# Kernel tuning notes

Hardware: AMD Instinct MI355X
Metric: run time of the kernel (lower is better)

Reference implementation:

```python
import jax, jax.numpy as jnp
import numpy as np

EMB = 256
N_NODES = 20000
N_EDGES = 200000


def _sage_layer(x, src, dst, edge_attr, W, b, n_nodes):
    # message = x[src] + edge_attr ; mean-aggregate into dst ; ReLU(Linear([x;agg]))
    msg = x[src] + edge_attr                                   # [2E, emb]
    s = jax.ops.segment_sum(msg, dst, num_segments=n_nodes)    # [N, emb]
    cnt = jax.ops.segment_sum(jnp.ones((dst.shape[0], 1), x.dtype), dst,
                              num_segments=n_nodes)            # [N, 1]
    agg = s / jnp.maximum(cnt, 1.0)
    return jax.nn.relu(jnp.concatenate([x, agg], axis=1) @ W + b)


def setup_inputs() -> dict:
    key = jax.random.key(0)
    ks = jax.random.split(key, 12)
    sc = 0.05
    inp = {
        "x": jax.random.normal(ks[0], (N_NODES, EMB), jnp.float32),
        "edge_attr": jax.random.normal(ks[1], (N_EDGES, EMB), jnp.float32),
        "batch_q_embds": jax.random.normal(ks[2], (N_EDGES, EMB), jnp.float32),
        "edge_index": jax.random.randint(ks[3], (2, N_EDGES), 0, N_NODES, jnp.int64
                                         if jax.config.jax_enable_x64 else jnp.int32),
        "W_rev1": jax.random.normal(ks[4], (EMB, EMB), jnp.float32) * sc,
        "b_rev1": jnp.zeros((EMB,), jnp.float32),
        "W_rev2": jax.random.normal(ks[5], (EMB, EMB), jnp.float32) * sc,
        "b_rev2": jnp.zeros((EMB,), jnp.float32),
        "W_sage1": jax.random.normal(ks[6], (2 * EMB, EMB), jnp.float32) * sc,
        "b_sage1": jnp.zeros((EMB,), jnp.float32),
        "W_sage2": jax.random.normal(ks[7], (2 * EMB, EMB), jnp.float32) * sc,
        "b_sage2": jnp.zeros((EMB,), jnp.float32),
        "W_pred1": jax.random.normal(ks[8], (6 * EMB, EMB), jnp.float32) * sc,
        "b_pred1": jnp.zeros((EMB,), jnp.float32),
        "W_pred2": jax.random.normal(ks[9], (EMB, 1), jnp.float32) * sc,
        "b_pred2": jnp.zeros((1,), jnp.float32),
    }
    return inp


def reference(x, edge_attr, batch_q_embds, edge_index,
              W_rev1, b_rev1, W_rev2, b_rev2,
              W_sage1, b_sage1, W_sage2, b_sage2,
              W_pred1, b_pred1, W_pred2, b_pred2):
    src, dst = edge_index[0], edge_index[1]
    # reverse-edge attributes via proj_reverse MLP
    edge_attr_rev = jax.nn.relu(edge_attr @ W_rev1 + b_rev1) @ W_rev2 + b_rev2
    src_f = jnp.concatenate([src, dst])          # [2E]
    dst_f = jnp.concatenate([dst, src])          # [2E]
    ea_f = jnp.concatenate([edge_attr, edge_attr_rev], axis=0)  # [2E, emb]
    # 2-layer GraphSAGE backbone over nodes, collect per-layer outputs
    h1 = _sage_layer(x, src_f, dst_f, ea_f, W_sage1, b_sage1, N_NODES)
    h2 = _sage_layer(h1, src_f, dst_f, ea_f, W_sage2, b_sage2, N_NODES)
    h_e = jnp.concatenate([h1, h2], axis=1)      # [N, 2*emb]
    # per-edge triple features: [q ; h_e[head] ; edge_attr ; h_e[tail]]
    h_triple = jnp.concatenate([batch_q_embds, h_e[src], edge_attr, h_e[dst]], axis=1)
    attn_logits = (jax.nn.relu(h_triple @ W_pred1 + b_pred1) @ W_pred2 + b_pred2)[:, 0]
    # idp-bern sampling (training=True): gumbel-like logistic noise, temp=1
    u = jax.random.uniform(jax.random.key(42), attn_logits.shape,
                           attn_logits.dtype, 1e-10, 1.0 - 1e-10)
    noise = jnp.log(u) - jnp.log(1.0 - u)
    sampled = jax.nn.sigmoid(attn_logits + noise)
    return attn_logits, sampled
```

## Files before the change

### kernel.cpp

```cpp
#include <hip/hip_runtime.h>
#include <cstdint>
#include <cstddef>

#define EMB 256
#define NN 20000
#define NE 200000
#define NE2 400000

typedef unsigned short ushort_t;
typedef __attribute__((ext_vector_type(8))) short bf16x8;
typedef __attribute__((ext_vector_type(4))) float f32x4;

__device__ __forceinline__ ushort_t f2bf(float f) {
    unsigned u = __float_as_uint(f);
    u += 0x7FFFu + ((u >> 16) & 1u);
    return (ushort_t)(u >> 16);
}
__device__ __forceinline__ float bf2f(ushort_t u) {
    return __uint_as_float(((unsigned)u) << 16);
}

__device__ __forceinline__ void async_cp16(const ushort_t* g, ushort_t* l) {
    __builtin_amdgcn_global_load_lds(
        (const __attribute__((address_space(1))) unsigned int*)g,
        (__attribute__((address_space(3))) unsigned int*)l,
        16, 0, 0);
}

__device__ __forceinline__ unsigned rotl32(unsigned v, int d) {
    return (v << d) | (v >> (32 - d));
}
__device__ __forceinline__ void threefry2x32(unsigned k0, unsigned k1,
                                             unsigned x0, unsigned x1,
                                             unsigned& o0, unsigned& o1) {
    unsigned k2 = k0 ^ k1 ^ 0x1BD11BDAu;
    x0 += k0; x1 += k1;
#define TF_R(r) { x0 += x1; x1 = rotl32(x1, (r)); x1 ^= x0; }
    TF_R(13) TF_R(15) TF_R(26) TF_R(6)
    x0 += k1; x1 += k2 + 1u;
    TF_R(17) TF_R(29) TF_R(16) TF_R(24)
    x0 += k2; x1 += k0 + 2u;
    TF_R(13) TF_R(15) TF_R(26) TF_R(6)
    x0 += k0; x1 += k1 + 3u;
    TF_R(17) TF_R(29) TF_R(16) TF_R(24)
    x0 += k1; x1 += k2 + 4u;
    TF_R(13) TF_R(15) TF_R(26) TF_R(6)
    x0 += k2; x1 += k0 + 5u;
#undef TF_R
    o0 = x0; o1 = x1;
}

__global__ void deg_kernel(const int* __restrict__ src, const int* __restrict__ dst,
                           int* __restrict__ deg) {
    int i = blockIdx.x * blockDim.x + threadIdx.x;
    if (i < NE2) {
        int n = (i < NE) ? dst[i] : src[i - NE];
        atomicAdd(&deg[n], 1);
    }
}

__global__ void prefix_kernel(const int* __restrict__ deg, int* __restrict__ row_start,
                              int* __restrict__ cursor) {
    __shared__ int sums[1024];
    int t = threadIdx.x;
    const int CH = (NN + 1023) / 1024;
    int lo = t * CH, hi = lo + CH;
    if (hi > NN) hi = NN;
    if (lo > NN) lo = NN;
    int s = 0;
    for (int n = lo; n < hi; n++) s += deg[n];
    sums[t] = s;
    __syncthreads();
    for (int off = 1; off < 1024; off <<= 1) {
        int v = (t >= off) ? sums[t - off] : 0;
        __syncthreads();
        sums[t] += v;
        __syncthreads();
    }
    int run = (t == 0) ? 0 : sums[t - 1];
    for (int n = lo; n < hi; n++) {
        row_start[n] = run;
        cursor[n] = run;
        run += deg[n];
    }
    if (t == 1023) row_start[NN] = sums[1023];
}

__global__ void scatter_kernel(const int* __restrict__ src, const int* __restrict__ dst,
                               int* __restrict__ cursor, int* __restrict__ elist) {
    int i = blockIdx.x * blockDim.x + threadIdx.x;
    if (i < NE2) {
        int n = (i < NE) ? dst[i] : src[i - NE];
        int pos = atomicAdd(&cursor[n], 1);
        elist[pos] = i;
    }
}

__global__ void conv2_kernel(const float* __restrict__ a, ushort_t* __restrict__ oa, int na8,
                             const float* __restrict__ b, ushort_t* __restrict__ ob, int nb8) {
    int i = blockIdx.x * 256 + threadIdx.x;
    const float* p;
    ushort_t* o;
    if (i < na8) { p = a + (size_t)i * 8; o = oa + (size_t)i * 8; }
    else {
        int j = i - na8;
        if (j >= nb8) return;
        p = b + (size_t)j * 8; o = ob + (size_t)j * 8;
    }
    float4 u = *(const float4*)p;
    float4 v = *(const float4*)(p + 4);
    union { ushort_t s[8]; uint4 w; } r;
    r.s[0] = f2bf(u.x); r.s[1] = f2bf(u.y); r.s[2] = f2bf(u.z); r.s[3] = f2bf(u.w);
    r.s[4] = f2bf(v.x); r.s[5] = f2bf(v.y); r.s[6] = f2bf(v.z); r.s[7] = f2bf(v.w);
    *(uint4*)o = r.w;
}

struct TD { const float* src; ushort_t* dst; int stride, koff, kr; };
struct TA { TD d[8]; };

__global__ void transpose_all_kernel(TA ta) {
    TD t = ta.d[blockIdx.y];
    int k = blockIdx.x;
    if (k >= t.kr) return;
    int n = threadIdx.x;
    t.dst[(size_t)n * t.stride + t.koff + k] = f2bf(t.src[(size_t)k * 256 + n]);
}

template <int KTOT, int EPI>
__global__ __launch_bounds__(256, 3) void mfma_gemm(
        const ushort_t* __restrict__ A0, int rsA0,
        const ushort_t* __restrict__ A1, int rsA1,
        const ushort_t* __restrict__ Bt, const ushort_t* __restrict__ Bt2,
        const float* __restrict__ bias,
        void* __restrict__ out, void* __restrict__ out2, int rsOut, int M,
        const int* __restrict__ srcp, const int* __restrict__ dstp,
        const float* __restrict__ Hs, const float* __restrict__ Hd,
        const float* __restrict__ w2) {
    __shared__ ushort_t As[128 * 32];
    __shared__ ushort_t Bs[128 * 32];
    __shared__ float red[128];

    int tid = threadIdx.x;
    int lane = tid & 63;
    int wave = tid >> 6;
    int wr = wave >> 1;
    int wc = wave & 1;
    int quad = lane >> 4;
    int col_l = lane & 15;
    int p = blockIdx.x >> 1;
    int colblk = blockIdx.x & 1;

    const ushort_t* Bsel = blockIdx.y ? Bt2 : Bt;
    void* Osel = blockIdx.y ? out2 : out;

    f32x4 acc[4][4];
#pragma unroll
    for (int mt = 0; mt < 4; mt++)
#pragma unroll
        for (int nt = 0; nt < 4; nt++) acc[mt][nt] = (f32x4)0.f;

    for (int k0 = 0; k0 < KTOT; k0 += 32) {
        __syncthreads();
        {
            const ushort_t* abase;
            int rs, koffs;
            if (KTOT == 512 && k0 >= 256) { abase = A1; rs = rsA1; koffs = k0 - 256; }
            else                          { abase = A0; rs = rsA0; koffs = k0; }
#pragma unroll
            for (int j = 0; j < 2; j++) {
                int flat = tid + 256 * j;
                int row = flat >> 2, ch = flat & 3;
                int grow = p * 128 + row;
                if (grow >= M) grow = M - 1;
                const ushort_t* gp = abase + (size_t)grow * rs + koffs + ch * 8;
                ushort_t* lp = As + ((wave * 64 + 256 * j) * 8);
                async_cp16(gp, lp);
            }
#pragma unroll
            for (int j = 0; j < 2; j++) {
                int flat = tid + 256 * j;
                int n = flat >> 2, ch = flat & 3;
                const ushort_t* gp = Bsel + (size_t)(colblk * 128 + n) * KTOT + k0 + ch * 8;
                ushort_t* lp = Bs + ((wave * 64 + 256 * j) * 8);
                async_cp16(gp, lp);
            }
        }
        __syncthreads();

        bf16x8 a[4], b[4];
#pragma unroll
        for (int mt = 0; mt < 4; mt++)
            a[mt] = *(const bf16x8*)(As + (wr * 64 + mt * 16 + col_l) * 32 + quad * 8);
#pragma unroll
        for (int nt = 0; nt < 4; nt++)
            b[nt] = *(const bf16x8*)(Bs + (wc * 64 + nt * 16 + col_l) * 32 + quad * 8);
#pragma unroll
        for (int mt = 0; mt < 4; mt++)
#pragma unroll
            for (int nt = 0; nt < 4; nt++)
                acc[mt][nt] = __builtin_amdgcn_mfma_f32_16x16x32_bf16(
                    a[mt], b[nt], acc[mt][nt], 0, 0, 0);
    }

    if (EPI == 4) {
        __syncthreads();
        if (tid < 128) red[tid] = 0.f;
        __syncthreads();
        float b1c[4], w2c[4];
#pragma unroll
        for (int nt = 0; nt < 4; nt++) {
            int col = colblk * 128 + wc * 64 + nt * 16 + col_l;
            b1c[nt] = bias[col];
            w2c[nt] = w2[col];
        }
#pragma unroll
        for (int mt = 0; mt < 4; mt++) {
#pragma unroll
            for (int r = 0; r < 4; r++) {
                int lrow = wr * 64 + mt * 16 + quad * 4 + r;
                int e = p * 128 + lrow;
                int ec = e < M ? e : M - 1;
                int s = srcp[ec], d = dstp[ec];
                const float* hsr = Hs + (size_t)s * 256;
                const float* hdr = Hd + (size_t)d * 256;
                float part = 0.f;
#pragma unroll
                for (int nt = 0; nt < 4; nt++) {
                    int col = colblk * 128 + wc * 64 + nt * 16 + col_l;
                    part += fmaxf(acc[mt][nt][r] + hsr[col] + hdr[col] + b1c[nt], 0.f)
                            * w2c[nt];
                }
#pragma unroll
                for (int m = 8; m > 0; m >>= 1) part += __shfl_xor(part, m, 64);
                if (col_l == 0) atomicAdd(&red[lrow], part);
            }
        }
        __syncthreads();
        if (tid < 128) {
            int e = p * 128 + tid;
            if (e < M) {
                float* tgt = colblk ? (float*)out2 : (float*)out;
                tgt[e] = red[tid];
            }
        }
        return;
    }

    float bs[4];
    if (EPI >= 2) {
#pragma unroll
        for (int nt = 0; nt < 4; nt++)
            bs[nt] = bias[colblk * 128 + wc * 64 + nt * 16 + col_l];
    }
#pragma unroll
    for (int mt = 0; mt < 4; mt++) {
#pragma unroll
        for (int nt = 0; nt < 4; nt++) {
            int colg = colblk * 128 + wc * 64 + nt * 16 + col_l;
#pragma unroll
            for (int r = 0; r < 4; r++) {
                int rg = p * 128 + wr * 64 + mt * 16 + quad * 4 + r;
                if (rg < M) {
                    float v = acc[mt][nt][r];
                    if (EPI >= 2) v += bs[nt];
                    if (EPI == 3) v = fmaxf(v, 0.f);
                    if (EPI == 0)
                        ((float*)Osel)[(size_t)rg * rsOut + colg] = v;
                    else
                        ((ushort_t*)Osel)[(size_t)rg * rsOut + colg] = f2bf(v);
                }
            }
        }
    }
}

__global__ void finalize_kernel(float* __restrict__ out, const float* __restrict__ part1,
                                const float* __restrict__ b2v, float* __restrict__ out_s) {
    int e = blockIdx.x * blockDim.x + threadIdx.x;
    if (e >= NE) return;
    float logit = out[e] + part1[e] + b2v[0];
    out[e] = logit;
    unsigned y0, y1;
    threefry2x32(0u, 42u, 0u, (unsigned)e, y0, y1);
    unsigned bits = y0 ^ y1;
    float f = __uint_as_float((bits >> 9) | 0x3F800000u) - 1.0f;
    float u = fmaxf(1e-10f, f + 1e-10f);
    float noise = logf(u) - logf(1.0f - u);
    out_s[e] = 1.0f / (1.0f + expf(-(logit + noise)));
}

__global__ __launch_bounds__(64) void agg_bf_kernel(
        const ushort_t* __restrict__ xin, int rsx,
        const ushort_t* __restrict__ eaf, const ushort_t* __restrict__ ear,
        const int* __restrict__ src, const int* __restrict__ dst,
        const int* __restrict__ row_start, const int* __restrict__ elist,
        const int* __restrict__ deg, ushort_t* __restrict__ agg) {
    int n = blockIdx.x;
    int c = threadIdx.x * 4;
    float ax = 0.f, ay = 0.f, az = 0.f, aw = 0.f;
    int beg = row_start[n], end = row_start[n + 1];
    for (int p = beg; p < end; p++) {
        int i = elist[p];
        const ushort_t* xr;
        const ushort_t* er;
        if (i < NE) { xr = xin + (size_t)src[i] * rsx; er = eaf + (size_t)i * 256; }
        else { int j = i - NE; xr = xin + (size_t)dst[j] * rsx; er = ear + (size_t)j * 256; }
        ushort4 xv = *(const ushort4*)(xr + c);
        ushort4 ev = *(const ushort4*)(er + c);
        ax += bf2f(xv.x) + bf2f(ev.x);
        ay += bf2f(xv.y) + bf2f(ev.y);
        az += bf2f(xv.z) + bf2f(ev.z);
        aw += bf2f(xv.w) + bf2f(ev.w);
    }
    float d = fmaxf((float)deg[n], 1.0f);
    ushort4 o;
    o.x = f2bf(ax / d); o.y = f2bf(ay / d); o.z = f2bf(az / d); o.w = f2bf(aw / d);
    *(ushort4*)(agg + (size_t)n * 256 + c) = o;
}

extern "C" void kernel_launch(void* const* d_in, const int* in_sizes, int n_in,
                              void* d_out, int out_size, void* d_ws, size_t ws_size,
                              hipStream_t stream) {
    const float* x        = (const float*)d_in[0];
    const float* ea       = (const float*)d_in[1];
    const float* qemb     = (const float*)d_in[2];
    const int*   eidx     = (const int*)d_in[3];
    const float* W_rev1   = (const float*)d_in[4];
    const float* b_rev1   = (const float*)d_in[5];
    const float* W_rev2   = (const float*)d_in[6];
    const float* b_rev2   = (const float*)d_in[7];
    const float* W_sage1  = (const float*)d_in[8];
    const float* b_sage1  = (const float*)d_in[9];
    const float* W_sage2  = (const float*)d_in[10];
    const float* b_sage2  = (const float*)d_in[11];
    const float* W_pred1  = (const float*)d_in[12];
    const float* b_pred1  = (const float*)d_in[13];
    const float* W_pred2  = (const float*)d_in[14];
    const float* b_pred2  = (const float*)d_in[15];
    float* out = (float*)d_out;

    const int* src = eidx;
    const int* dst = eidx + NE;

    char* w = (char*)d_ws;
    ushort_t* ea_bf  = (ushort_t*)w; w += (size_t)NE * 256 * 2;
    ushort_t* hid_bf = (ushort_t*)w; w += (size_t)NE * 256 * 2;
    ushort_t* ea_rev_bf = (ushort_t*)w; w += (size_t)NE * 256 * 2;
    ushort_t* x_bf   = (ushort_t*)w; w += (size_t)NN * 256 * 2;
    ushort_t* H      = (ushort_t*)w; w += (size_t)NN * 512 * 2;
    ushort_t* agg_bf = (ushort_t*)w; w += (size_t)NN * 256 * 2;
    float*    Hsrc   = (float*)w;    w += (size_t)NN * 256 * 4;
    float*    Hdst   = (float*)w;    w += (size_t)NN * 256 * 4;
    float*    part1  = (float*)w;    w += (size_t)NE * 4;
    ushort_t* Wt_rev1  = (ushort_t*)w; w += 256 * 256 * 2;
    ushort_t* Wt_rev2  = (ushort_t*)w; w += 256 * 256 * 2;
    ushort_t* Wt_sage1 = (ushort_t*)w; w += 256 * 512 * 2;
    ushort_t* Wt_sage2 = (ushort_t*)w; w += 256 * 512 * 2;
    ushort_t* Wt_src   = (ushort_t*)w; w += 256 * 512 * 2;
    ushort_t* Wt_dst   = (ushort_t*)w; w += 256 * 512 * 2;
    ushort_t* Wt_edge  = (ushort_t*)w; w += 256 * 512 * 2;
    int* deg       = (int*)w; w += (size_t)NN * 4;
    int* row_start = (int*)w; w += (size_t)(NN + 1) * 4;
    int* cursor    = (int*)w; w += (size_t)NN * 4;
    int* elist     = (int*)w; w += (size_t)NE2 * 4;

    const int EB = (NE + 127) / 128;
    const int NB = (NN + 127) / 128;

    hipMemsetAsync(deg, 0, (size_t)NN * 4, stream);
    deg_kernel<<<(NE2 + 255) / 256, 256, 0, stream>>>(src, dst, deg);
    prefix_kernel<<<1, 1024, 0, stream>>>(deg, row_start, cursor);
    scatter_kernel<<<(NE2 + 255) / 256, 256, 0, stream>>>(src, dst, cursor, elist);

    TA ta;
    ta.d[0] = { W_rev1,  Wt_rev1,  256, 0,   256 };
    ta.d[1] = { W_rev2,  Wt_rev2,  256, 0,   256 };
    ta.d[2] = { W_sage1, Wt_sage1, 512, 0,   512 };
    ta.d[3] = { W_sage2, Wt_sage2, 512, 0,   512 };
    ta.d[4] = { W_pred1 + (size_t)256 * 256,  Wt_src,  512, 0,   512 };
    ta.d[5] = { W_pred1 + (size_t)1024 * 256, Wt_dst,  512, 0,   512 };
    ta.d[6] = { W_pred1,                      Wt_edge, 512, 0,   256 };
    ta.d[7] = { W_pred1 + (size_t)768 * 256,  Wt_edge, 512, 256, 256 };
    transpose_all_kernel<<<dim3(512, 8), 256, 0, stream>>>(ta);

    conv2_kernel<<<((NE + NN) * 32 + 255) / 256, 256, 0, stream>>>(
        ea, ea_bf, NE * 32, x, x_bf, NN * 32);

    mfma_gemm<256, 3><<<EB * 2, 256, 0, stream>>>(
        ea_bf, 256, nullptr, 0, Wt_rev1, nullptr, b_rev1,
        hid_bf, nullptr, 256, NE, nullptr, nullptr, nullptr, nullptr, nullptr);
    mfma_gemm<256, 2><<<EB * 2, 256, 0, stream>>>(
        hid_bf, 256, nullptr, 0, Wt_rev2, nullptr, b_rev2,
        ea_rev_bf, nullptr, 256, NE, nullptr, nullptr, nullptr, nullptr, nullptr);

    conv2_kernel<<<(NE * 32 + 255) / 256, 256, 0, stream>>>(
        qemb, hid_bf, NE * 32, qemb, hid_bf, 0);

    agg_bf_kernel<<<NN, 64, 0, stream>>>(x_bf, 256, ea_bf, ea_rev_bf,
                                         src, dst, row_start, elist, deg, agg_bf);
    mfma_gemm<512, 3><<<NB * 2, 256, 0, stream>>>(
        x_bf, 256, agg_bf, 256, Wt_sage1, nullptr, b_sage1,
        H, nullptr, 512, NN, nullptr, nullptr, nullptr, nullptr, nullptr);

    agg_bf_kernel<<<NN, 64, 0, stream>>>(H, 512, ea_bf, ea_rev_bf,
                                         src, dst, row_start, elist, deg, agg_bf);
    mfma_gemm<512, 3><<<NB * 2, 256, 0, stream>>>(
        H, 512, agg_bf, 256, Wt_sage2, nullptr, b_sage2,
        H + 256, nullptr, 512, NN, nullptr, nullptr, nullptr, nullptr, nullptr);

    mfma_gemm<512, 0><<<dim3(NB * 2, 2), 256, 0, stream>>>(
        H, 512, H + 256, 512, Wt_src, Wt_dst, nullptr,
        Hsrc, Hdst, 256, NN, nullptr, nullptr, nullptr, nullptr, nullptr);

    mfma_gemm<512, 4><<<EB * 2, 256, 0, stream>>>(
        hid_bf, 256, ea_bf, 256, Wt_edge, nullptr, b_pred1,
        out, part1, 0, NE, src, dst, Hsrc, Hdst, W_pred2);

    finalize_kernel<<<(NE + 255) / 256, 256, 0, stream>>>(out, part1, b_pred2, out + NE);
}
```

Before: 1.025 ms.

## Fuse reverse-edge MLP into one kernel, convert qemb in GEMM, remap blocks

Replaces the two reverse-projection GEMMs with one fused kernel. It keeps the ReLU hidden tile in LDS as bf16 and runs the second GEMM from there, so the 200k x 256 hidden intermediate never goes to global memory. The separate fp32-to-bf16 conversion of the query embeddings is removed: the final edge GEMM now loads fp32 qemb and converts it while staging into shared memory. A block-index remapping groups row and column blocks for better cache locality. The fused kernel uses more LDS and registers (launch bounds of 2), which lowers occupancy, and the fp32 A loads are synchronous rather than async.

```diff
diff --git a/kernel.cpp b/kernel.cpp
--- a/kernel.cpp
+++ b/kernel.cpp
@@ -25,6 +25,19 @@
         (const __attribute__((address_space(1))) unsigned int*)g,
         (__attribute__((address_space(3))) unsigned int*)l,
         16, 0, 0);
+}
+
+__device__ __forceinline__ void pc_map(int bid, int T, int& p, int& colblk) {
+    int Tf = T & ~15;
+    if (bid < Tf) {
+        p = (bid >> 4) * 8 + (bid & 7);
+        colblk = (bid >> 3) & 1;
+    } else {
+        int rem = bid - Tf;
+        int nr = (T - Tf) >> 1;
+        p = (T >> 1) - nr + rem % nr;
+        colblk = rem / nr;
+    }
 }
 
 __device__ __forceinline__ unsigned rotl32(unsigned v, int d) {
@@ -126,9 +139,149 @@
     t.dst[(size_t)n * t.stride + t.koff + k] = f2bf(t.src[(size_t)k * 256 + n]);
 }
 
-template <int KTOT, int EPI>
+__global__ __launch_bounds__(256, 2) void rev_fused_kernel(
+        const ushort_t* __restrict__ ea_bf,
+        const ushort_t* __restrict__ Wt1, const float* __restrict__ b1,
+        const ushort_t* __restrict__ Wt2, const float* __restrict__ b2,
+        ushort_t* __restrict__ ea_rev) {
+    __shared__ ushort_t As[128 * 32];
+    __shared__ ushort_t Bs[256 * 32];
+    __shared__ ushort_t Hl[128 * 136];
+
+    int tid = threadIdx.x;
+    int lane = tid & 63, wave = tid >> 6;
+    int wr = wave >> 1, wc = wave & 1;
+    int quad = lane >> 4, col_l = lane & 15;
+    int p = blockIdx.x;
+
+    f32x4 acc[4][8];
+#pragma unroll
+    for (int mt = 0; mt < 4; mt++)
+#pragma unroll
+        for (int nt = 0; nt < 8; nt++) acc[mt][nt] = (f32x4)0.f;
+
+    for (int k0 = 0; k0 < 256; k0 += 32) {
+        __syncthreads();
+#pragma unroll
+        for (int j = 0; j < 2; j++) {
+            int flat = tid + 256 * j;
+            int row = flat >> 2, ch = flat & 3;
+            int grow = p * 128 + row;
+            if (grow >= NE) grow = NE - 1;
+            async_cp16(ea_bf + (size_t)grow * 256 + k0 + ch * 8,
+                       As + (wave * 64 + 256 * j) * 8);
+        }
+#pragma unroll
+        for (int j = 0; j < 4; j++) {
+            int flat = tid + 256 * j;
+            int n = flat >> 2, ch = flat & 3;
+            async_cp16(Wt1 + (size_t)n * 256 + k0 + ch * 8,
+                       Bs + (wave * 64 + 256 * j) * 8);
+        }
+        __syncthreads();
+        bf16x8 a[4], b[8];
+#pragma unroll
+        for (int mt = 0; mt < 4; mt++)
+            a[mt] = *(const bf16x8*)(As + (wr * 64 + mt * 16 + col_l) * 32 + quad * 8);
+#pragma unroll
+        for (int nt = 0; nt < 8; nt++)
+            b[nt] = *(const bf16x8*)(Bs + (wc * 128 + nt * 16 + col_l) * 32 + quad * 8);
+#pragma unroll
+        for (int mt = 0; mt < 4; mt++)
+#pragma unroll
+            for (int nt = 0; nt < 8; nt++)
+                acc[mt][nt] = __builtin_amdgcn_mfma_f32_16x16x32_bf16(
+                    a[mt], b[nt], acc[mt][nt], 0, 0, 0);
+    }
+
+    unsigned hpk[4][8][2];
+#pragma unroll
+    for (int mt = 0; mt < 4; mt++)
+#pragma unroll
+        for (int nt = 0; nt < 8; nt++) {
+            float bb = b1[wc * 128 + nt * 16 + col_l];
+#pragma unroll
+            for (int j = 0; j < 2; j++) {
+                float f0 = fmaxf(acc[mt][nt][2 * j] + bb, 0.f);
+                float f1 = fmaxf(acc[mt][nt][2 * j + 1] + bb, 0.f);
+                hpk[mt][nt][j] = (unsigned)f2bf(f0) | ((unsigned)f2bf(f1) << 16);
+            }
+        }
+
+    f32x4 acc2[4][8];
+#pragma unroll
+    for (int mt = 0; mt < 4; mt++)
+#pragma unroll
+        for (int nt = 0; nt < 8; nt++) {
+            float bb = b2[wc * 128 + nt * 16 + col_l];
+            acc2[mt][nt] = (f32x4)0.f;
+            if (mt == 0) {
+            }
+            acc2[mt][nt][0] = (mt == 0) ? 0.f : 0.f;
+            (void)bb;
+        }
+
+    for (int hc = 0; hc < 2; hc++) {
+        __syncthreads();
+        if (wc == hc) {
+#pragma unroll
+            for (int mt = 0; mt < 4; mt++)
+#pragma unroll
+                for (int nt = 0; nt < 8; nt++)
+#pragma unroll
+                    for (int j = 0; j < 2; j++) {
+                        int row = wr * 64 + mt * 16 + quad * 4 + 2 * j;
+                        int cc = nt * 16 + col_l;
+                        unsigned u = hpk[mt][nt][j];
+                        Hl[row * 136 + cc] = (ushort_t)u;
+                        Hl[(row + 1) * 136 + cc] = (ushort_t)(u >> 16);
+                    }
+        }
+        for (int kk = 0; kk < 4; kk++) {
+            __syncthreads();
+#pragma unroll
+            for (int j = 0; j < 4; j++) {
+                int flat = tid + 256 * j;
+                int n = flat >> 2, ch = flat & 3;
+                async_cp16(Wt2 + (size_t)n * 256 + hc * 128 + kk * 32 + ch * 8,
+                           Bs + (wave * 64 + 256 * j) * 8);
+            }
+            __syncthreads();
+            bf16x8 a[4], b[8];
+#pragma unroll
+            for (int mt = 0; mt < 4; mt++)
+                a[mt] = *(const bf16x8*)(Hl + (wr * 64 + mt * 16 + col_l) * 136
+                                         + kk * 32 + quad * 8);
+#pragma unroll
+            for (int nt = 0; nt < 8; nt++)
+                b[nt] = *(const bf16x8*)(Bs + (wc * 128 + nt * 16 + col_l) * 32 + quad * 8);
+#pragma unroll
+            for (int mt = 0; mt < 4; mt++)
+#pragma unroll
+                for (int nt = 0; nt < 8; nt++)
+                    acc2[mt][nt] = __builtin_amdgcn_mfma_f32_16x16x32_bf16(
+                        a[mt], b[nt], acc2[mt][nt], 0, 0, 0);
+        }
+    }
+
+#pragma unroll
+    for (int mt = 0; mt < 4; mt++)
+#pragma unroll
+        for (int nt = 0; nt < 8; nt++) {
+            int colg = wc * 128 + nt * 16 + col_l;
+            float bb = b2[colg];
+#pragma unroll
+            for (int r = 0; r < 4; r++) {
+                int rg = p * 128 + wr * 64 + mt * 16 + quad * 4 + r;
+                if (rg < NE)
+                    ea_rev[(size_t)rg * 256 + colg] = f2bf(acc2[mt][nt][r] + bb);
+            }
+        }
+}
+
+template <int KTOT, int EPI, bool A0F32>
 __global__ __launch_bounds__(256, 3) void mfma_gemm(
-        const ushort_t* __restrict__ A0, int rsA0,
+        const void* __restrict__ A0v, int rsA0,
         const ushort_t* __restrict__ A1, int rsA1,
         const ushort_t* __restrict__ Bt, const ushort_t* __restrict__ Bt2,
         const float* __restrict__ bias,
@@ -147,8 +300,8 @@
     int wc = wave & 1;
     int quad = lane >> 4;
     int col_l = lane & 15;
-    int p = blockIdx.x >> 1;
-    int colblk = blockIdx.x & 1;
+    int p, colblk;
+    pc_map(blockIdx.x, gridDim.x, p, colblk);
 
     const ushort_t* Bsel = blockIdx.y ? Bt2 : Bt;
     void* Osel = blockIdx.y ? out2 : out;
@@ -161,11 +314,34 @@
 
     for (int k0 = 0; k0 < KTOT; k0 += 32) {
         __syncthreads();
-        {
+#pragma unroll
+        for (int j = 0; j < 2; j++) {
+            int flat = tid + 256 * j;
+            int n = flat >> 2, ch = flat & 3;
+            const ushort_t* gp = Bsel + (size_t)(colblk * 128 + n) * KTOT + k0 + ch * 8;
+            async_cp16(gp, Bs + ((wave * 64 + 256 * j) * 8));
+        }
+        bool seg1 = (KTOT == 512) && (k0 >= 256);
+        if (A0F32 && !seg1) {
+#pragma unroll
+            for (int j = 0; j < 2; j++) {
+                int flat = tid + 256 * j;
+                int row = flat >> 2, ch = flat & 3;
+                int grow = p * 128 + row;
+                if (grow >= M) grow = M - 1;
+                const float* gp = (const float*)A0v + (size_t)grow * rsA0 + k0 + ch * 8;
+                float4 u = *(const float4*)gp;
+                float4 v = *(const float4*)(gp + 4);
+                union { ushort_t s[8]; uint4 w; } r;
+                r.s[0] = f2bf(u.x); r.s[1] = f2bf(u.y); r.s[2] = f2bf(u.z); r.s[3] = f2bf(u.w);
+                r.s[4] = f2bf(v.x); r.s[5] = f2bf(v.y); r.s[6] = f2bf(v.z); r.s[7] = f2bf(v.w);
+                *(uint4*)(As + (size_t)flat * 8) = r.w;
+            }
+        } else {
             const ushort_t* abase;
             int rs, koffs;
             if (KTOT == 512 && k0 >= 256) { abase = A1; rs = rsA1; koffs = k0 - 256; }
-            else                          { abase = A0; rs = rsA0; koffs = k0; }
+            else { abase = (const ushort_t*)A0v; rs = rsA0; koffs = k0; }
 #pragma unroll
             for (int j = 0; j < 2; j++) {
                 int flat = tid + 256 * j;
@@ -173,16 +349,7 @@
                 int grow = p * 128 + row;
                 if (grow >= M) grow = M - 1;
                 const ushort_t* gp = abase + (size_t)grow * rs + koffs + ch * 8;
-                ushort_t* lp = As + ((wave * 64 + 256 * j) * 8);
-                async_cp16(gp, lp);
-            }
-#pragma unroll
-            for (int j = 0; j < 2; j++) {
-                int flat = tid + 256 * j;
-                int n = flat >> 2, ch = flat & 3;
-                const ushort_t* gp = Bsel + (size_t)(colblk * 128 + n) * KTOT + k0 + ch * 8;
-                ushort_t* lp = Bs + ((wave * 64 + 256 * j) * 8);
-                async_cp16(gp, lp);
+                async_cp16(gp, As + ((wave * 64 + 256 * j) * 8));
             }
         }
         __syncthreads();
@@ -344,7 +511,6 @@
 
     char* w = (char*)d_ws;
     ushort_t* ea_bf  = (ushort_t*)w; w += (size_t)NE * 256 * 2;
-    ushort_t* hid_bf = (ushort_t*)w; w += (size_t)NE * 256 * 2;
     ushort_t* ea_rev_bf = (ushort_t*)w; w += (size_t)NE * 256 * 2;
     ushort_t* x_bf   = (ushort_t*)w; w += (size_t)NN * 256 * 2;
     ushort_t* H      = (ushort_t*)w; w += (size_t)NN * 512 * 2;
@@ -386,34 +552,27 @@
     conv2_kernel<<<((NE + NN) * 32 + 255) / 256, 256, 0, stream>>>(
         ea, ea_bf, NE * 32, x, x_bf, NN * 32);
 
-    mfma_gemm<256, 3><<<EB * 2, 256, 0, stream>>>(
-        ea_bf, 256, nullptr, 0, Wt_rev1, nullptr, b_rev1,
-        hid_bf, nullptr, 256, NE, nullptr, nullptr, nullptr, nullptr, nullptr);
-    mfma_gemm<256, 2><<<EB * 2, 256, 0, stream>>>(
-        hid_bf, 256, nullptr, 0, Wt_rev2, nullptr, b_rev2,
-        ea_rev_bf, nullptr, 256, NE, nullptr, nullptr, nullptr, nullptr, nullptr);
-
-    conv2_kernel<<<(NE * 32 + 255) / 256, 256, 0, stream>>>(
-        qemb, hid_bf, NE * 32, qemb, hid_bf, 0);
+    rev_fused_kernel<<<EB, 256, 0, stream>>>(
+        ea_bf, Wt_rev1, b_rev1, Wt_rev2, b_rev2, ea_rev_bf);
 
     agg_bf_kernel<<<NN, 64, 0, stream>>>(x_bf, 256, ea_bf, ea_rev_bf,
                                          src, dst, row_start, elist, deg, agg_bf);
-    mfma_gemm<512, 3><<<NB * 2, 256, 0, stream>>>(
+    mfma_gemm<512, 3, false><<<NB * 2, 256, 0, stream>>>(
         x_bf, 256, agg_bf, 256, Wt_sage1, nullptr, b_sage1,
         H, nullptr, 512, NN, nullptr, nullptr, nullptr, nullptr, nullptr);
 
     agg_bf_kernel<<<NN, 64, 0, stream>>>(H, 512, ea_bf, ea_rev_bf,
                                          src, dst, row_start, elist, deg, agg_bf);
-    mfma_gemm<512, 3><<<NB * 2, 256, 0, stream>>>(
+    mfma_gemm<512, 3, false><<<NB * 2, 256, 0, stream>>>(
         H, 512, agg_bf, 256, Wt_sage2, nullptr, b_sage2,
         H + 256, nullptr, 512, NN, nullptr, nullptr, nullptr, nullptr, nullptr);
 
-    mfma_gemm<512, 0><<<dim3(NB * 2, 2), 256, 0, stream>>>(
+    mfma_gemm<512, 0, false><<<dim3(NB * 2, 2), 256, 0, stream>>>(
         H, 512, H + 256, 512, Wt_src, Wt_dst, nullptr,
         Hsrc, Hdst, 256, NN, nullptr, nullptr, nullptr, nullptr, nullptr);
 
-    mfma_gemm<512, 4><<<EB * 2, 256, 0, stream>>>(
-        hid_bf, 256, ea_bf, 256, Wt_edge, nullptr, b_pred1,
+    mfma_gemm<512, 4, true><<<EB * 2, 256, 0, stream>>>(
+        qemb, 256, ea_bf, 256, Wt_edge, nullptr, b_pred1,
         out, part1, 0, NE, src, dst, Hsrc, Hdst, W_pred2);
 
     finalize_kernel<<<(NE + 255) / 256, 256, 0, stream>>>(out, part1, b_pred2, out + NE);
```

Result: slower. 1.084 ms (+5.8%).

## Fuse qemb fp32 conversion into GEMM, split aggregation, remap GEMM block order

Applied to the files above, without the earlier changes.

The final edge GEMM now reads batch_q_embds directly in fp32 and converts it to bf16 while staging A tiles, which removes a separate conversion pass and its bf16 round trip. The edge-attribute aggregation, identical in both SAGE layers, is computed once into an fp32 buffer (aliasing Hsrc), and each layer then gathers only node features. GEMM blocks are also remapped so groups of row tiles share column-block B data, aiming for better cache locality. The fp32 A path uses synchronous loads instead of async LDS copies, which may add latency in that GEMM.

```diff
diff --git a/kernel.cpp b/kernel.cpp
--- a/kernel.cpp
+++ b/kernel.cpp
@@ -25,6 +25,19 @@
         (const __attribute__((address_space(1))) unsigned int*)g,
         (__attribute__((address_space(3))) unsigned int*)l,
         16, 0, 0);
+}
+
+__device__ __forceinline__ void pc_map(int bid, int T, int& p, int& colblk) {
+    int Tf = T & ~15;
+    if (bid < Tf) {
+        p = (bid >> 4) * 8 + (bid & 7);
+        colblk = (bid >> 3) & 1;
+    } else {
+        int rem = bid - Tf;
+        int nr = (T - Tf) >> 1;
+        p = (T >> 1) - nr + rem % nr;
+        colblk = rem / nr;
+    }
 }
 
 __device__ __forceinline__ unsigned rotl32(unsigned v, int d) {
@@ -126,9 +139,9 @@
     t.dst[(size_t)n * t.stride + t.koff + k] = f2bf(t.src[(size_t)k * 256 + n]);
 }
 
-template <int KTOT, int EPI>
+template <int KTOT, int EPI, bool A0F32>
 __global__ __launch_bounds__(256, 3) void mfma_gemm(
-        const ushort_t* __restrict__ A0, int rsA0,
+        const void* __restrict__ A0v, int rsA0,
         const ushort_t* __restrict__ A1, int rsA1,
         const ushort_t* __restrict__ Bt, const ushort_t* __restrict__ Bt2,
         const float* __restrict__ bias,
@@ -147,8 +160,8 @@
     int wc = wave & 1;
     int quad = lane >> 4;
     int col_l = lane & 15;
-    int p = blockIdx.x >> 1;
-    int colblk = blockIdx.x & 1;
+    int p, colblk;
+    pc_map(blockIdx.x, gridDim.x, p, colblk);
 
     const ushort_t* Bsel = blockIdx.y ? Bt2 : Bt;
     void* Osel = blockIdx.y ? out2 : out;
@@ -161,11 +174,34 @@
 
     for (int k0 = 0; k0 < KTOT; k0 += 32) {
         __syncthreads();
-        {
+#pragma unroll
+        for (int j = 0; j < 2; j++) {
+            int flat = tid + 256 * j;
+            int n = flat >> 2, ch = flat & 3;
+            const ushort_t* gp = Bsel + (size_t)(colblk * 128 + n) * KTOT + k0 + ch * 8;
+            async_cp16(gp, Bs + ((wave * 64 + 256 * j) * 8));
+        }
+        bool seg1 = (KTOT == 512) && (k0 >= 256);
+        if (A0F32 && !seg1) {
+#pragma unroll
+            for (int j = 0; j < 2; j++) {
+                int flat = tid + 256 * j;
+                int row = flat >> 2, ch = flat & 3;
+                int grow = p * 128 + row;
+                if (grow >= M) grow = M - 1;
+                const float* gp = (const float*)A0v + (size_t)grow * rsA0 + k0 + ch * 8;
+                float4 u = *(const float4*)gp;
+                float4 v = *(const float4*)(gp + 4);
+                union { ushort_t s[8]; uint4 w; } r;
+                r.s[0] = f2bf(u.x); r.s[1] = f2bf(u.y); r.s[2] = f2bf(u.z); r.s[3] = f2bf(u.w);
+                r.s[4] = f2bf(v.x); r.s[5] = f2bf(v.y); r.s[6] = f2bf(v.z); r.s[7] = f2bf(v.w);
+                *(uint4*)(As + (size_t)flat * 8) = r.w;
+            }
+        } else {
             const ushort_t* abase;
             int rs, koffs;
             if (KTOT == 512 && k0 >= 256) { abase = A1; rs = rsA1; koffs = k0 - 256; }
-            else                          { abase = A0; rs = rsA0; koffs = k0; }
+            else { abase = (const ushort_t*)A0v; rs = rsA0; koffs = k0; }
 #pragma unroll
             for (int j = 0; j < 2; j++) {
                 int flat = tid + 256 * j;
@@ -173,16 +209,7 @@
                 int grow = p * 128 + row;
                 if (grow >= M) grow = M - 1;
                 const ushort_t* gp = abase + (size_t)grow * rs + koffs + ch * 8;
-                ushort_t* lp = As + ((wave * 64 + 256 * j) * 8);
-                async_cp16(gp, lp);
-            }
-#pragma unroll
-            for (int j = 0; j < 2; j++) {
-                int flat = tid + 256 * j;
-                int n = flat >> 2, ch = flat & 3;
-                const ushort_t* gp = Bsel + (size_t)(colblk * 128 + n) * KTOT + k0 + ch * 8;
-                ushort_t* lp = Bs + ((wave * 64 + 256 * j) * 8);
-                async_cp16(gp, lp);
+                async_cp16(gp, As + ((wave * 64 + 256 * j) * 8));
             }
         }
         __syncthreads();
@@ -289,32 +316,46 @@
     out_s[e] = 1.0f / (1.0f + expf(-(logit + noise)));
 }
 
-__global__ __launch_bounds__(64) void agg_bf_kernel(
-        const ushort_t* __restrict__ xin, int rsx,
+__global__ __launch_bounds__(64) void agg_ea_kernel(
         const ushort_t* __restrict__ eaf, const ushort_t* __restrict__ ear,
-        const int* __restrict__ src, const int* __restrict__ dst,
         const int* __restrict__ row_start, const int* __restrict__ elist,
-        const int* __restrict__ deg, ushort_t* __restrict__ agg) {
+        float* __restrict__ agg_ea) {
     int n = blockIdx.x;
     int c = threadIdx.x * 4;
     float ax = 0.f, ay = 0.f, az = 0.f, aw = 0.f;
     int beg = row_start[n], end = row_start[n + 1];
     for (int p = beg; p < end; p++) {
         int i = elist[p];
-        const ushort_t* xr;
-        const ushort_t* er;
-        if (i < NE) { xr = xin + (size_t)src[i] * rsx; er = eaf + (size_t)i * 256; }
-        else { int j = i - NE; xr = xin + (size_t)dst[j] * rsx; er = ear + (size_t)j * 256; }
-        ushort4 xv = *(const ushort4*)(xr + c);
+        const ushort_t* er = (i < NE) ? eaf + (size_t)i * 256
+                                      : ear + (size_t)(i - NE) * 256;
         ushort4 ev = *(const ushort4*)(er + c);
-        ax += bf2f(xv.x) + bf2f(ev.x);
-        ay += bf2f(xv.y) + bf2f(ev.y);
-        az += bf2f(xv.z) + bf2f(ev.z);
-        aw += bf2f(xv.w) + bf2f(ev.w);
-    }
+        ax += bf2f(ev.x); ay += bf2f(ev.y); az += bf2f(ev.z); aw += bf2f(ev.w);
+    }
+    float4 o; o.x = ax; o.y = ay; o.z = az; o.w = aw;
+    *(float4*)(agg_ea + (size_t)n * 256 + c) = o;
+}
+
+__global__ __launch_bounds__(64) void agg_x_kernel(
+        const ushort_t* __restrict__ xin, int rsx,
+        const int* __restrict__ src, const int* __restrict__ dst,
+        const int* __restrict__ row_start, const int* __restrict__ elist,
+        const int* __restrict__ deg, const float* __restrict__ agg_ea,
+        ushort_t* __restrict__ agg) {
+    int n = blockIdx.x;
+    int c = threadIdx.x * 4;
+    float ax = 0.f, ay = 0.f, az = 0.f, aw = 0.f;
+    int beg = row_start[n], end = row_start[n + 1];
+    for (int p = beg; p < end; p++) {
+        int i = elist[p];
+        int node = (i < NE) ? src[i] : dst[i - NE];
+        ushort4 xv = *(const ushort4*)(xin + (size_t)node * rsx + c);
+        ax += bf2f(xv.x); ay += bf2f(xv.y); az += bf2f(xv.z); aw += bf2f(xv.w);
+    }
+    float4 e = *(const float4*)(agg_ea + (size_t)n * 256 + c);
     float d = fmaxf((float)deg[n], 1.0f);
     ushort4 o;
-    o.x = f2bf(ax / d); o.y = f2bf(ay / d); o.z = f2bf(az / d); o.w = f2bf(aw / d);
+    o.x = f2bf((ax + e.x) / d); o.y = f2bf((ay + e.y) / d);
+    o.z = f2bf((az + e.z) / d); o.w = f2bf((aw + e.w) / d);
     *(ushort4*)(agg + (size_t)n * 256 + c) = o;
 }
 
@@ -364,6 +405,8 @@
     int* cursor    = (int*)w; w += (size_t)NN * 4;
     int* elist     = (int*)w; w += (size_t)NE2 * 4;
 
+    float* agg_ea = Hsrc;
+
     const int EB = (NE + 127) / 128;
     const int NB = (NN + 127) / 128;
 
@@ -386,34 +429,33 @@
     conv2_kernel<<<((NE + NN) * 32 + 255) / 256, 256, 0, stream>>>(
         ea, ea_bf, NE * 32, x, x_bf, NN * 32);
 
-    mfma_gemm<256, 3><<<EB * 2, 256, 0, stream>>>(
+    mfma_gemm<256, 3, false><<<EB * 2, 256, 0, stream>>>(
         ea_bf, 256, nullptr, 0, Wt_rev1, nullptr, b_rev1,
         hid_bf, nullptr, 256, NE, nullptr, nullptr, nullptr, nullptr, nullptr);
-    mfma_gemm<256, 2><<<EB * 2, 256, 0, stream>>>(
+    mfma_gemm<256, 2, false><<<EB * 2, 256, 0, stream>>>(
         hid_bf, 256, nullptr, 0, Wt_rev2, nullptr, b_rev2,
         ea_rev_bf, nullptr, 256, NE, nullptr, nullptr, nullptr, nullptr, nullptr);
 
-    conv2_kernel<<<(NE * 32 + 255) / 256, 256, 0, stream>>>(
-        qemb, hid_bf, NE * 32, qemb, hid_bf, 0);
-
-    agg_bf_kernel<<<NN, 64, 0, stream>>>(x_bf, 256, ea_bf, ea_rev_bf,
-                                         src, dst, row_start, elist, deg, agg_bf);
-    mfma_gemm<512, 3><<<NB * 2, 256, 0, stream>>>(
+    agg_ea_kernel<<<NN, 64, 0, stream>>>(ea_bf, ea_rev_bf, row_start, elist, agg_ea);
+
+    agg_x_kernel<<<NN, 64, 0, stream>>>(x_bf, 256, src, dst, row_start, elist,
+                                        deg, agg_ea, agg_bf);
+    mfma_gemm<512, 3, false><<<NB * 2, 256, 0, stream>>>(
         x_bf, 256, agg_bf, 256, Wt_sage1, nullptr, b_sage1,
         H, nullptr, 512, NN, nullptr, nullptr, nullptr, nullptr, nullptr);
 
-    agg_bf_kernel<<<NN, 64, 0, stream>>>(H, 512, ea_bf, ea_rev_bf,
-                                         src, dst, row_start, elist, deg, agg_bf);
-    mfma_gemm<512, 3><<<NB * 2, 256, 0, stream>>>(
+    agg_x_kernel<<<NN, 64, 0, stream>>>(H, 512, src, dst, row_start, elist,
+                                        deg, agg_ea, agg_bf);
+    mfma_gemm<512, 3, false><<<NB * 2, 256, 0, stream>>>(
         H, 512, agg_bf, 256, Wt_sage2, nullptr, b_sage2,
         H + 256, nullptr, 512, NN, nullptr, nullptr, nullptr, nullptr, nullptr);
 
-    mfma_gemm<512, 0><<<dim3(NB * 2, 2), 256, 0, stream>>>(
+    mfma_gemm<512, 0, false><<<dim3(NB * 2, 2), 256, 0, stream>>>(
         H, 512, H + 256, 512, Wt_src, Wt_dst, nullptr,
         Hsrc, Hdst, 256, NN, nullptr, nullptr, nullptr, nullptr, nullptr);
 
-    mfma_gemm<512, 4><<<EB * 2, 256, 0, stream>>>(
-        hid_bf, 256, ea_bf, 256, Wt_edge, nullptr, b_pred1,
+    mfma_gemm<512, 4, true><<<EB * 2, 256, 0, stream>>>(
+        qemb, 256, ea_bf, 256, Wt_edge, nullptr, b_pred1,
         out, part1, 0, NE, src, dst, Hsrc, Hdst, W_pred2);
 
     finalize_kernel<<<(NE + 255) / 256, 256, 0, stream>>>(out, part1, b_pred2, out + NE);
```

Measured after the change: 983.1 us. -4.1%, faster.
